# Kernel tuning notes

Measured on AMD Instinct MI355X. Metric: run time of the kernel, lower is better.

## Reference

```python
import jax, jax.numpy as jnp
import numpy as np

SMOOTHNESS_WEIGHT = 0.01
TRANSITION_PENALTY_WEIGHT = 0.1
NUM_CLASSES = 3

B, C, T = 512, 3, 16384


def setup_inputs() -> dict:
    key = jax.random.key(0)
    k1, k2 = jax.random.split(key)
    logits = jax.random.normal(k1, (B, C, T), dtype=jnp.float32)
    labels = jax.random.randint(k2, (B, T), 0, NUM_CLASSES, dtype=jnp.int64)
    return {"logits": logits, "labels": labels}


def reference(logits, labels):
    # --- cross entropy (mean over all B*T positions), logits [B, C, T] ---
    logp = jax.nn.log_softmax(logits, axis=1)                      # [B, C, T]
    nll = -jnp.take_along_axis(logp, labels[:, None, :], axis=1)   # [B, 1, T]
    ce = jnp.mean(nll)

    # --- smoothness: mean squared temporal difference of logits ---
    diff = jnp.mean((logits[:, :, 1:] - logits[:, :, :-1]) ** 2)
    smoothness_penalty = SMOOTHNESS_WEIGHT * diff

    # --- transition penalty: mean penalty over invalid (prev, next) pairs ---
    preds = jnp.argmax(logits, axis=1)                             # [B, T]
    # penalty lookup table: invalid transitions (0->2), (2->1), (1->0) = 1
    table = (jnp.zeros((NUM_CLASSES, NUM_CLASSES), dtype=jnp.float32)
             .at[0, 2].set(1.0).at[2, 1].set(1.0).at[1, 0].set(1.0))
    vals = table[preds[:, :-1], preds[:, 1:]]                      # [B, T-1]
    count = jnp.sum(vals > 0)
    # mean over invalid transitions only; 0.0 if none occur
    transition_penalty = TRANSITION_PENALTY_WEIGHT * jnp.where(
        count > 0, jnp.sum(vals) / jnp.maximum(count, 1).astype(vals.dtype), 0.0)

    return ce + smoothness_penalty + transition_penalty
```

## Files before the change

### kernel.cpp

```cpp
#include <hip/hip_runtime.h>

#define BB 512
#define CC 3
#define TT 16384

#define NBLK 2048
#define NTHREADS (NBLK * 256)
#define NQUAD (BB * TT / 4)
#define ITERS (NQUAD / NTHREADS)

__global__ __launch_bounds__(256) void ce_trans_main(const float* __restrict__ logits,
                                                     const int* __restrict__ labels,
                                                     float* __restrict__ partials) {
    float nll = 0.f, ss = 0.f;
    int cnt = 0;

#pragma unroll
    for (int it = 0; it < ITERS; ++it) {
        const int q  = it * NTHREADS + blockIdx.x * 256 + threadIdx.x;
        const int b  = q >> 12;
        const int tq = q & 4095;
        const int t0 = tq << 2;

        const float* p0 = logits + (size_t)b * (CC * TT) + t0;
        const float4 a4 = *reinterpret_cast<const float4*>(p0);
        const float4 b4 = *reinterpret_cast<const float4*>(p0 + TT);
        const float4 c4 = *reinterpret_cast<const float4*>(p0 + 2 * TT);
        const int4   l4 = *reinterpret_cast<const int4*>(labels + (size_t)b * TT + t0);

        float x0[5] = {a4.x, a4.y, a4.z, a4.w, 0.f};
        float x1[5] = {b4.x, b4.y, b4.z, b4.w, 0.f};
        float x2[5] = {c4.x, c4.y, c4.z, c4.w, 0.f};
        const bool hasNext = (tq != 4095);
        if (hasNext) {
            x0[4] = p0[4];
            x1[4] = p0[TT + 4];
            x2[4] = p0[2 * TT + 4];
        }
        const int lab[4] = {l4.x, l4.y, l4.z, l4.w};

        int am[5];
#pragma unroll
        for (int j = 0; j < 5; ++j) {
            const float v0 = x0[j], v1 = x1[j], v2 = x2[j];
            int idx = 0;
            float mx = v0;
            if (v1 > mx) { mx = v1; idx = 1; }
            if (v2 > mx) { mx = v2; idx = 2; }
            am[j] = idx;
            if (j < 4) {
                const float e   = __expf(v0 - mx) + __expf(v1 - mx) + __expf(v2 - mx);
                const float lse = mx + __logf(e);
                const float xl  = (lab[j] == 0) ? v0 : ((lab[j] == 1) ? v1 : v2);
                nll += lse - xl;
            }
        }

        const int nd = hasNext ? 4 : 3;
#pragma unroll
        for (int j = 0; j < 4; ++j) {
            if (j < nd) {
                const float d0 = x0[j + 1] - x0[j];
                const float d1 = x1[j + 1] - x1[j];
                const float d2 = x2[j + 1] - x2[j];
                ss += d0 * d0 + d1 * d1 + d2 * d2;
                cnt += (am[j + 1] == ((am[j] + 2) % 3)) ? 1 : 0;
            }
        }
    }

    float fcnt = (float)cnt;
#pragma unroll
    for (int off = 32; off > 0; off >>= 1) {
        nll  += __shfl_down(nll,  off, 64);
        ss   += __shfl_down(ss,   off, 64);
        fcnt += __shfl_down(fcnt, off, 64);
    }

    __shared__ float s_nll[4], s_ss[4], s_cnt[4];
    const int wave = threadIdx.x >> 6;
    const int lane = threadIdx.x & 63;
    if (lane == 0) { s_nll[wave] = nll; s_ss[wave] = ss; s_cnt[wave] = fcnt; }
    __syncthreads();
    if (threadIdx.x == 0) {
        partials[blockIdx.x]            = s_nll[0] + s_nll[1] + s_nll[2] + s_nll[3];
        partials[NBLK + blockIdx.x]     = s_ss[0]  + s_ss[1]  + s_ss[2]  + s_ss[3];
        partials[2 * NBLK + blockIdx.x] = s_cnt[0] + s_cnt[1] + s_cnt[2] + s_cnt[3];
    }
}

__global__ __launch_bounds__(256) void ce_trans_final(const float* __restrict__ partials,
                                                      float* __restrict__ out) {
    float sn = 0.f, st = 0.f, sc = 0.f;
    for (int i = threadIdx.x; i < NBLK; i += 256) {
        sn += partials[i];
        st += partials[NBLK + i];
        sc += partials[2 * NBLK + i];
    }
#pragma unroll
    for (int off = 32; off > 0; off >>= 1) {
        sn += __shfl_down(sn, off, 64);
        st += __shfl_down(st, off, 64);
        sc += __shfl_down(sc, off, 64);
    }
    __shared__ float s_n[4], s_s[4], s_c[4];
    const int wave = threadIdx.x >> 6;
    const int lane = threadIdx.x & 63;
    if (lane == 0) { s_n[wave] = sn; s_s[wave] = st; s_c[wave] = sc; }
    __syncthreads();
    if (threadIdx.x == 0) {
        const float tn = s_n[0] + s_n[1] + s_n[2] + s_n[3];
        const float ts = s_s[0] + s_s[1] + s_s[2] + s_s[3];
        const float tc = s_c[0] + s_c[1] + s_c[2] + s_c[3];
        const float ce = tn / 8388608.0f;
        const float sm = 0.01f * (ts / 25164288.0f);
        const float tp = (tc > 0.5f) ? 0.1f : 0.0f;
        out[0] = ce + sm + tp;
    }
}

extern "C" void kernel_launch(void* const* d_in, const int* in_sizes, int n_in,
                              void* d_out, int out_size, void* d_ws, size_t ws_size,
                              hipStream_t stream) {
    const float* logits = (const float*)d_in[0];
    const int*   labels = (const int*)d_in[1];
    float* out      = (float*)d_out;
    float* partials = (float*)d_ws;

    ce_trans_main<<<NBLK, 256, 0, stream>>>(logits, labels, partials);
    ce_trans_final<<<1, 256, 0, stream>>>(partials, out);
}
```

Baseline: 173.9 us.

## Double-buffer nontemporal loads and fetch neighbor logits via wave shuffles

The main loop now issues the next iteration's logits and labels loads before computing the current one, using two register slots so memory latency overlaps compute. Loads are marked nontemporal. The per-thread scalar loads of the next timestep are replaced by a wave shuffle from the neighbouring lane, with only lane 63 reading global memory. The transition check becomes a bitmask lookup, and the final reduction reads partials as float4. The aim is fewer redundant uncoalesced scalar loads and better latency hiding, at the cost of more registers.

```diff
diff --git a/kernel.cpp b/kernel.cpp
--- a/kernel.cpp
+++ b/kernel.cpp
@@ -1,9 +1,11 @@
 #include <hip/hip_runtime.h>
+
+typedef float v4f __attribute__((ext_vector_type(4)));
+typedef int   v4i __attribute__((ext_vector_type(4)));
 
 #define BB 512
 #define CC 3
 #define TT 16384
-
 #define NBLK 2048
 #define NTHREADS (NBLK * 256)
 #define NQUAD (BB * TT / 4)
@@ -12,61 +14,93 @@
 __global__ __launch_bounds__(256) void ce_trans_main(const float* __restrict__ logits,
                                                      const int* __restrict__ labels,
                                                      float* __restrict__ partials) {
+    const int tid0 = blockIdx.x * 256 + threadIdx.x;
+    const int lane = threadIdx.x & 63;
+
     float nll = 0.f, ss = 0.f;
     int cnt = 0;
 
-#pragma unroll
-    for (int it = 0; it < ITERS; ++it) {
-        const int q  = it * NTHREADS + blockIdx.x * 256 + threadIdx.x;
+    v4f A[2], Bv[2], Cv[2];
+    v4i Lv[2];
+    int TQ[2];
+    const float* P0[2];
+
+    auto issue = [&](int it, int slot) {
+        const int q  = it * NTHREADS + tid0;
         const int b  = q >> 12;
         const int tq = q & 4095;
-        const int t0 = tq << 2;
+        const float* p0 = logits + (size_t)b * (CC * TT) + (tq << 2);
+        A[slot]  = __builtin_nontemporal_load((const v4f*)p0);
+        Bv[slot] = __builtin_nontemporal_load((const v4f*)(p0 + TT));
+        Cv[slot] = __builtin_nontemporal_load((const v4f*)(p0 + 2 * TT));
+        Lv[slot] = __builtin_nontemporal_load((const v4i*)(labels + (size_t)b * TT + (tq << 2)));
+        TQ[slot] = tq;
+        P0[slot] = p0;
+    };
 
-        const float* p0 = logits + (size_t)b * (CC * TT) + t0;
-        const float4 a4 = *reinterpret_cast<const float4*>(p0);
-        const float4 b4 = *reinterpret_cast<const float4*>(p0 + TT);
-        const float4 c4 = *reinterpret_cast<const float4*>(p0 + 2 * TT);
-        const int4   l4 = *reinterpret_cast<const int4*>(labels + (size_t)b * TT + t0);
+    auto compute = [&](int slot) {
+        const v4f a = A[slot], bq = Bv[slot], c = Cv[slot];
+        const v4i l = Lv[slot];
+        const float x0[4] = {a.x,  a.y,  a.z,  a.w};
+        const float x1[4] = {bq.x, bq.y, bq.z, bq.w};
+        const float x2[4] = {c.x,  c.y,  c.z,  c.w};
+        const int  lab[4] = {l.x,  l.y,  l.z,  l.w};
+        int am[4];
 
-        float x0[5] = {a4.x, a4.y, a4.z, a4.w, 0.f};
-        float x1[5] = {b4.x, b4.y, b4.z, b4.w, 0.f};
-        float x2[5] = {c4.x, c4.y, c4.z, c4.w, 0.f};
-        const bool hasNext = (tq != 4095);
-        if (hasNext) {
-            x0[4] = p0[4];
-            x1[4] = p0[TT + 4];
-            x2[4] = p0[2 * TT + 4];
-        }
-        const int lab[4] = {l4.x, l4.y, l4.z, l4.w};
-
-        int am[5];
 #pragma unroll
-        for (int j = 0; j < 5; ++j) {
+        for (int j = 0; j < 4; ++j) {
             const float v0 = x0[j], v1 = x1[j], v2 = x2[j];
             int idx = 0;
             float mx = v0;
             if (v1 > mx) { mx = v1; idx = 1; }
             if (v2 > mx) { mx = v2; idx = 2; }
             am[j] = idx;
-            if (j < 4) {
-                const float e   = __expf(v0 - mx) + __expf(v1 - mx) + __expf(v2 - mx);
-                const float lse = mx + __logf(e);
-                const float xl  = (lab[j] == 0) ? v0 : ((lab[j] == 1) ? v1 : v2);
-                nll += lse - xl;
+            const float e  = __expf(v0 - mx) + __expf(v1 - mx) + __expf(v2 - mx);
+            const float xl = (lab[j] == 0) ? v0 : ((lab[j] == 1) ? v1 : v2);
+            nll += mx + __logf(e) - xl;
+        }
+
+#pragma unroll
+        for (int j = 0; j < 3; ++j) {
+            const float d0 = x0[j + 1] - x0[j];
+            const float d1 = x1[j + 1] - x1[j];
+            const float d2 = x2[j + 1] - x2[j];
+            ss += d0 * d0 + d1 * d1 + d2 * d2;
+            cnt += (0x8C >> (3 * am[j] + am[j + 1])) & 1;
+        }
+
+        float xn0 = __shfl_down(x0[0], 1, 64);
+        float xn1 = __shfl_down(x1[0], 1, 64);
+        float xn2 = __shfl_down(x2[0], 1, 64);
+        int   amn = __shfl_down(am[0], 1, 64);
+        bool valid = true;
+        if (lane == 63) {
+            if (TQ[slot] == 4095) {
+                valid = false;
+            } else {
+                const float* p0 = P0[slot];
+                xn0 = p0[4]; xn1 = p0[TT + 4]; xn2 = p0[2 * TT + 4];
+                int idx = 0;
+                float mx = xn0;
+                if (xn1 > mx) { mx = xn1; idx = 1; }
+                if (xn2 > mx) { mx = xn2; idx = 2; }
+                amn = idx;
             }
         }
+        if (valid) {
+            const float d0 = xn0 - x0[3];
+            const float d1 = xn1 - x1[3];
+            const float d2 = xn2 - x2[3];
+            ss += d0 * d0 + d1 * d1 + d2 * d2;
+            cnt += (0x8C >> (3 * am[3] + amn)) & 1;
+        }
+    };
 
-        const int nd = hasNext ? 4 : 3;
+    issue(0, 0);
 #pragma unroll
-        for (int j = 0; j < 4; ++j) {
-            if (j < nd) {
-                const float d0 = x0[j + 1] - x0[j];
-                const float d1 = x1[j + 1] - x1[j];
-                const float d2 = x2[j + 1] - x2[j];
-                ss += d0 * d0 + d1 * d1 + d2 * d2;
-                cnt += (am[j + 1] == ((am[j] + 2) % 3)) ? 1 : 0;
-            }
-        }
+    for (int it = 0; it < ITERS; ++it) {
+        if (it + 1 < ITERS) issue(it + 1, (it + 1) & 1);
+        compute(it & 1);
     }
 
     float fcnt = (float)cnt;
@@ -79,8 +113,7 @@
 
     __shared__ float s_nll[4], s_ss[4], s_cnt[4];
     const int wave = threadIdx.x >> 6;
-    const int lane = threadIdx.x & 63;
-    if (lane == 0) { s_nll[wave] = nll; s_ss[wave] = ss; s_cnt[wave] = fcnt; }
+    if ((threadIdx.x & 63) == 0) { s_nll[wave] = nll; s_ss[wave] = ss; s_cnt[wave] = fcnt; }
     __syncthreads();
     if (threadIdx.x == 0) {
         partials[blockIdx.x]            = s_nll[0] + s_nll[1] + s_nll[2] + s_nll[3];
@@ -92,10 +125,15 @@
 __global__ __launch_bounds__(256) void ce_trans_final(const float* __restrict__ partials,
                                                       float* __restrict__ out) {
     float sn = 0.f, st = 0.f, sc = 0.f;
-    for (int i = threadIdx.x; i < NBLK; i += 256) {
-        sn += partials[i];
-        st += partials[NBLK + i];
-        sc += partials[2 * NBLK + i];
+#pragma unroll
+    for (int k = 0; k < 2; ++k) {
+        const int i = k * 256 + threadIdx.x;
+        const v4f n4 = *((const v4f*)partials + i);
+        const v4f s4 = *((const v4f*)partials + 512 + i);
+        const v4f c4 = *((const v4f*)partials + 1024 + i);
+        sn += n4.x + n4.y + n4.z + n4.w;
+        st += s4.x + s4.y + s4.z + s4.w;
+        sc += c4.x + c4.y + c4.z + c4.w;
     }
 #pragma unroll
     for (int off = 32; off > 0; off >>= 1) {
@@ -105,8 +143,7 @@
     }
     __shared__ float s_n[4], s_s[4], s_c[4];
     const int wave = threadIdx.x >> 6;
-    const int lane = threadIdx.x & 63;
-    if (lane == 0) { s_n[wave] = sn; s_s[wave] = st; s_c[wave] = sc; }
+    if ((threadIdx.x & 63) == 0) { s_n[wave] = sn; s_s[wave] = st; s_c[wave] = sc; }
     __syncthreads();
     if (threadIdx.x == 0) {
         const float tn = s_n[0] + s_n[1] + s_n[2] + s_n[3];
```

After: 167.8 us. 3.5% less time.
